# Kernel tuning notes

Measured on AMD Instinct MI355X. Metric: run time of the kernel, lower is better.

Reference implementation:

```python
import jax, jax.numpy as jnp
import numpy as np

ALPHA_MEM = 0.95      # util.decayconst(tau_mem)
ALPHA_MEM_OUT = 0.95  # util.decayconst(tau_mem_out)
ALPHA_P = 0.99        # util.decayconst(tau_p)
SURR_SCALE = 100.0

@jax.custom_vjp
def spike(x):
    # Heaviside forward, surrogate gradient backward (SurrGradSpike)
    return (x > 0).astype(x.dtype)

def _spike_fwd(x):
    return spike(x), x

def _spike_bwd(x, g):
    return (g / (SURR_SCALE * jnp.abs(x) + 1.0) ** 2,)

spike.defvjp(_spike_fwd, _spike_bwd)


def setup_inputs() -> dict:
    B, T, N, NIN, NOUT, D = 64, 400, 1024, 128, 32, 3
    key = jax.random.key(0)
    ks = jax.random.split(key, 8)
    inputs = jax.random.normal(ks[0], (B, T, NIN), dtype=jnp.float32)
    w = jax.random.normal(ks[1], (N, N), dtype=jnp.float32) / np.sqrt(N).astype(np.float32)
    w_in = jax.random.normal(ks[2], (NIN, N), dtype=jnp.float32) * np.float32(0.3 / np.sqrt(NIN))
    w_out = jax.random.normal(ks[3], (N, NOUT), dtype=jnp.float32) * np.float32(0.3 / np.sqrt(N))
    w_signs = jnp.where(jax.random.uniform(ks[4], (N,)) < 0.8, 1.0, -1.0).astype(jnp.float32)
    dmap = (jax.random.uniform(ks[5], (D, N, N)) < 0.2).astype(jnp.float32)  # delay-wise connectivity mask
    p = jax.random.uniform(ks[6], (N,), minval=-0.5, maxval=0.5).astype(jnp.float32)
    delays = jnp.array([1, 2, 4], dtype=jnp.int32)
    return dict(inputs=inputs, w=w, w_in=w_in, w_out=w_out, w_signs=w_signs,
                dmap=dmap, p=p, delays=delays)


def _forward(inputs, w, w_in, w_out, w_signs, dmap, p, delays):
    B, T, _ = inputs.shape
    N = w.shape[0]
    L = int(np.max(np.asarray(delays))) + 1  # ring-buffer length (static)
    dtype = inputs.dtype

    inp = jnp.einsum('btc,cn->btn', inputs, w_in)           # epoch.input, (B,T,N)
    W = dmap * (w_signs[:, None] * jnp.abs(w))[None]        # (D,N,N)
    depr = (p < 0).astype(dtype)                            # p_depr_mask

    def step(carry, inp_t):
        mem, w_p, buf_out, buf_wp, t = carry
        out = spike(mem - 1.0)                              # mark_spikes
        buf_out = buf_out.at[t % L].set(out)                # record_state
        buf_wp = buf_wp.at[t % L].set(w_p)
        idx = (t - delays) % L
        syn_p = buf_out[idx] * (1.0 + buf_wp[idx])          # (D,B,N)
        syn = jnp.einsum('dbe,deo->bo', syn_p, W)
        w_p_new = w_p * ALPHA_P + out * p * (1.0 + depr * w_p)
        mem_new = ALPHA_MEM * mem + inp_t + syn - jax.lax.stop_gradient(out)
        return (mem_new, w_p_new, buf_out, buf_wp, t + 1), out

    z = jnp.zeros((B, N), dtype)
    bufs = jnp.zeros((L, B, N), dtype)
    carry0 = (z, z, bufs, bufs, jnp.int32(0))
    _, out_rec = jax.lax.scan(step, carry0, jnp.swapaxes(inp, 0, 1))  # (T,B,N)

    # compute_readout: leaky integrator over projected spikes
    h2 = jnp.einsum('tbn,no->tbo', out_rec, w_out)
    def ro_step(r, h):
        r = ALPHA_MEM_OUT * r + h
        return r, r
    _, readout = jax.lax.scan(ro_step, jnp.zeros((B, w_out.shape[1]), dtype), h2)
    return jnp.swapaxes(readout, 0, 1)                      # (B,T,NOUT)


def reference(inputs, w, w_in, w_out, w_signs, dmap, p, delays):
    return _forward(inputs, w, w_in, w_out, w_signs, dmap, p, delays)
```

## Files before the change

### kernel.cpp

```cpp
#include <hip/hip_runtime.h>
#include <cstdint>
#include <cstddef>

#define BB    64
#define TT    400
#define NN    1024
#define NIN   128
#define NOUT  32
#define DD    3
#define LL6   6
#define GG    16
#define BPG   4
#define NT    32
#define KK    3072

#define ALPHA_MEM     0.95f
#define ALPHA_MEM_OUT 0.95f
#define ALPHA_P       0.99f

__global__ void build_W(const float* __restrict__ w,
                        const float* __restrict__ w_signs,
                        const float* __restrict__ dmap,
                        float* __restrict__ W) {
    int idx = blockIdx.x * blockDim.x + threadIdx.x;
    if (idx >= DD * NN * NN) return;
    int en = idx % (NN * NN);
    int e  = en / NN;
    W[idx] = dmap[idx] * (w_signs[e] * fabsf(w[en]));
}

__global__ void gemm_in(const float* __restrict__ inputs,
                        const float* __restrict__ w_in,
                        float* __restrict__ inp) {
    int idx = blockIdx.x * blockDim.x + threadIdx.x;
    if (idx >= TT * BB * NN) return;
    int n  = idx & (NN - 1);
    int tb = idx >> 10;
    int b  = tb & 63;
    int t  = tb >> 6;
    const float* row = inputs + ((size_t)b * TT + t) * NIN;
    float acc = 0.0f;
    #pragma unroll 8
    for (int c = 0; c < NIN; ++c)
        acc = fmaf(row[c], w_in[c * NN + n], acc);
    inp[idx] = acc;
}

__global__ void zero_sc1(float* __restrict__ p, int n) {
    int i = blockIdx.x * blockDim.x + threadIdx.x;
    if (i < n)
        __hip_atomic_store(p + i, 0.0f, __ATOMIC_RELAXED, __HIP_MEMORY_SCOPE_AGENT);
}

__global__ __launch_bounds__(256, 2) void snn_scan(
    const float* __restrict__ inputs,
    const float* __restrict__ w_in,
    const float* __restrict__ w_out,
    const float* __restrict__ p,
    const int*   __restrict__ delays,
    const float* __restrict__ W,
    const float* __restrict__ w_raw,
    const float* __restrict__ w_signs,
    const float* __restrict__ dmap,
    float*       __restrict__ ring,
    int*         __restrict__ cnt,
    float*       __restrict__ hpart,
    const float* __restrict__ inp_pre,
    float*       __restrict__ out,
    int use_pre, int use_W)
{
    __shared__ __align__(16) float sa[KK * BPG];
    __shared__ float w_out_s[32 * NOUT];
    __shared__ float spk_s[BPG * 32];
    __shared__ float s_sign[NN];
    __shared__ float s_in[BPG * NIN];

    const int bid  = blockIdx.x;
    const int g    = bid >> 5;
    const int tile = bid & 31;
    const int tid  = threadIdx.x;
    const int lane = tid & 63;
    const int wv   = tid >> 6;

    const bool st = (tid < BPG * 32);
    const int  sb = tid >> 5;
    const int  nl = tid & 31;

    const int gks = tid >> 3;
    const int gcg = tid & 7;

    float mem = 0.0f, wp = 0.0f, r = 0.0f;
    float pn = 0.0f, depr = 0.0f;
    if (st) { pn = p[tile * 32 + nl]; depr = (pn < 0.0f) ? 1.0f : 0.0f; }

    const int d0 = delays[0], d1 = delays[1], d2 = delays[2];

    for (int k = tid; k < 32 * NOUT; k += 256)
        w_out_s[k] = w_out[(tile * 32 + (k >> 5)) * NOUT + (k & 31)];
    if (!use_W)
        for (int k = tid; k < NN; k += 256) s_sign[k] = w_signs[k];
    __syncthreads();

    const float* Wt = W     + tile * 32 + gcg * 4;
    const float* Dt = dmap  + tile * 32 + gcg * 4;
    const float* Rt = w_raw + tile * 32 + gcg * 4;

    for (int t = 0; t < TT; ++t) {
        const int slot_w = t % LL6;
        const int s0 = (t - d0 + 2 * LL6) % LL6;
        const int s1 = (t - d1 + 2 * LL6) % LL6;
        const int s2 = (t - d2 + 2 * LL6) % LL6;

        bool  spk = false;
        float ia  = 0.0f;
        if (st) {
            spk = (mem - 1.0f) > 0.0f;
            const float a = spk ? (1.0f + wp) : 0.0f;
            __hip_atomic_store(ring + (((size_t)slot_w * BB + g * BPG + sb) << 10)
                                    + tile * 32 + nl,
                               a, __ATOMIC_RELAXED, __HIP_MEMORY_SCOPE_AGENT);
            wp = ALPHA_P * wp + (spk ? pn * (1.0f + depr * wp) : 0.0f);
            spk_s[tid] = spk ? 1.0f : 0.0f;
            if (use_pre)
                ia = inp_pre[((size_t)t * BB + g * BPG + sb) * NN + tile * 32 + nl];
        }
        if (!use_pre) {
            for (int k = tid; k < BPG * NIN; k += 256) {
                int b2 = k >> 7, c = k & 127;
                s_in[k] = inputs[((size_t)(g * BPG + b2) * TT + t) * NIN + c];
            }
        }
        __syncthreads();

        if (st) {
            float h = 0.0f;
            #pragma unroll
            for (int n2 = 0; n2 < 32; ++n2)
                h = fmaf(spk_s[sb * 32 + n2], w_out_s[n2 * 32 + nl], h);
            __hip_atomic_store(hpart + ((((size_t)(t & 1) * NT + tile) * BB)
                                        + g * BPG + sb) * NOUT + nl,
                               h, __ATOMIC_RELAXED, __HIP_MEMORY_SCOPE_AGENT);
            if (!use_pre) {
                #pragma unroll 8
                for (int c = 0; c < NIN; ++c)
                    ia = fmaf(s_in[sb * NIN + c], w_in[c * NN + tile * 32 + nl], ia);
            }
        }
        __syncthreads();

        if (tid == 0) {
            __hip_atomic_fetch_add(&cnt[g * 32], 1, __ATOMIC_RELEASE,
                                   __HIP_MEMORY_SCOPE_AGENT);
            const int target = 32 * (t + 1);
            while (__hip_atomic_load(&cnt[g * 32], __ATOMIC_RELAXED,
                                     __HIP_MEMORY_SCOPE_AGENT) < target)
                __builtin_amdgcn_s_sleep(2);
        }
        __syncthreads();

        if (tile == 0 && st) {
            float h = 0.0f;
            #pragma unroll
            for (int k3 = 0; k3 < NT; ++k3)
                h += __hip_atomic_load(hpart + ((((size_t)(t & 1) * NT + k3) * BB)
                                                + g * BPG + sb) * NOUT + nl,
                                       __ATOMIC_RELAXED, __HIP_MEMORY_SCOPE_AGENT);
            r = ALPHA_MEM_OUT * r + h;
            out[((size_t)(g * BPG + sb) * TT + t) * NOUT + nl] = r;
        }

        {
            const int b2 = lane >> 4;
            const int eo = lane & 15;
            #pragma unroll 16
            for (int i = 0; i < 48; ++i) {
                const int c  = i * 4 + wv;
                const int kl = c * 16 + eo;
                const int d  = kl >> 10;
                const int e  = kl & 1023;
                const int sl = (d == 0) ? s0 : ((d == 1) ? s1 : s2);
                const float v = __hip_atomic_load(
                    ring + (((size_t)sl * BB + g * BPG + b2) << 10) + e,
                    __ATOMIC_RELAXED, __HIP_MEMORY_SCOPE_AGENT);
                sa[kl * 4 + b2] = v;
            }
        }
        __syncthreads();

        float4 acc0 = {0,0,0,0}, acc1 = {0,0,0,0}, acc2 = {0,0,0,0}, acc3 = {0,0,0,0};
        if (use_W) {
            #pragma unroll 8
            for (int i = 0; i < 96; ++i) {
                const int kk = gks + (i << 5);
                const float4 av = *(const float4*)&sa[kk << 2];
                const float4 wv4 = *(const float4*)(Wt + ((size_t)kk << 10));
                acc0.x = fmaf(av.x, wv4.x, acc0.x); acc0.y = fmaf(av.x, wv4.y, acc0.y);
                acc0.z = fmaf(av.x, wv4.z, acc0.z); acc0.w = fmaf(av.x, wv4.w, acc0.w);
                acc1.x = fmaf(av.y, wv4.x, acc1.x); acc1.y = fmaf(av.y, wv4.y, acc1.y);
                acc1.z = fmaf(av.y, wv4.z, acc1.z); acc1.w = fmaf(av.y, wv4.w, acc1.w);
                acc2.x = fmaf(av.z, wv4.x, acc2.x); acc2.y = fmaf(av.z, wv4.y, acc2.y);
                acc2.z = fmaf(av.z, wv4.z, acc2.z); acc2.w = fmaf(av.z, wv4.w, acc2.w);
                acc3.x = fmaf(av.w, wv4.x, acc3.x); acc3.y = fmaf(av.w, wv4.y, acc3.y);
                acc3.z = fmaf(av.w, wv4.z, acc3.z); acc3.w = fmaf(av.w, wv4.w, acc3.w);
            }
        } else {
            #pragma unroll 2
            for (int i = 0; i < 96; ++i) {
                const int kk = gks + (i << 5);
                const int e  = kk & 1023;
                const float sg = s_sign[e];
                const float4 dm = *(const float4*)(Dt + ((size_t)kk << 10));
                const float4 wr = *(const float4*)(Rt + ((size_t)e << 10));
                float4 wv4;
                wv4.x = dm.x * (sg * fabsf(wr.x));
                wv4.y = dm.y * (sg * fabsf(wr.y));
                wv4.z = dm.z * (sg * fabsf(wr.z));
                wv4.w = dm.w * (sg * fabsf(wr.w));
                const float4 av = *(const float4*)&sa[kk << 2];
                acc0.x = fmaf(av.x, wv4.x, acc0.x); acc0.y = fmaf(av.x, wv4.y, acc0.y);
                acc0.z = fmaf(av.x, wv4.z, acc0.z); acc0.w = fmaf(av.x, wv4.w, acc0.w);
                acc1.x = fmaf(av.y, wv4.x, acc1.x); acc1.y = fmaf(av.y, wv4.y, acc1.y);
                acc1.z = fmaf(av.y, wv4.z, acc1.z); acc1.w = fmaf(av.y, wv4.w, acc1.w);
                acc2.x = fmaf(av.z, wv4.x, acc2.x); acc2.y = fmaf(av.z, wv4.y, acc2.y);
                acc2.z = fmaf(av.z, wv4.z, acc2.z); acc2.w = fmaf(av.z, wv4.w, acc2.w);
                acc3.x = fmaf(av.w, wv4.x, acc3.x); acc3.y = fmaf(av.w, wv4.y, acc3.y);
                acc3.z = fmaf(av.w, wv4.z, acc3.z); acc3.w = fmaf(av.w, wv4.w, acc3.w);
            }
        }
        __syncthreads();

        float* red = sa;
        {
            const int o0 = gcg * 4;
            red[(0 * 32 + o0 + 0) * 33 + gks] = acc0.x;
            red[(0 * 32 + o0 + 1) * 33 + gks] = acc0.y;
            red[(0 * 32 + o0 + 2) * 33 + gks] = acc0.z;
            red[(0 * 32 + o0 + 3) * 33 + gks] = acc0.w;
            red[(1 * 32 + o0 + 0) * 33 + gks] = acc1.x;
            red[(1 * 32 + o0 + 1) * 33 + gks] = acc1.y;
            red[(1 * 32 + o0 + 2) * 33 + gks] = acc1.z;
            red[(1 * 32 + o0 + 3) * 33 + gks] = acc1.w;
            red[(2 * 32 + o0 + 0) * 33 + gks] = acc2.x;
            red[(2 * 32 + o0 + 1) * 33 + gks] = acc2.y;
            red[(2 * 32 + o0 + 2) * 33 + gks] = acc2.z;
            red[(2 * 32 + o0 + 3) * 33 + gks] = acc2.w;
            red[(3 * 32 + o0 + 0) * 33 + gks] = acc3.x;
            red[(3 * 32 + o0 + 1) * 33 + gks] = acc3.y;
            red[(3 * 32 + o0 + 2) * 33 + gks] = acc3.z;
            red[(3 * 32 + o0 + 3) * 33 + gks] = acc3.w;
        }
        __syncthreads();

        if (st) {
            float syn = 0.0f;
            #pragma unroll
            for (int k2 = 0; k2 < 32; ++k2)
                syn += red[tid * 33 + k2];
            mem = ALPHA_MEM * mem + ia + syn - (spk ? 1.0f : 0.0f);
        }
        __syncthreads();
    }
}

extern "C" void kernel_launch(void* const* d_in, const int* in_sizes, int n_in,
                              void* d_out, int out_size, void* d_ws, size_t ws_size,
                              hipStream_t stream) {
    const float* inputs  = (const float*)d_in[0];
    const float* w       = (const float*)d_in[1];
    const float* w_in    = (const float*)d_in[2];
    const float* w_out   = (const float*)d_in[3];
    const float* w_signs = (const float*)d_in[4];
    const float* dmap    = (const float*)d_in[5];
    const float* p       = (const float*)d_in[6];
    const int*   delays  = (const int*)d_in[7];
    float*       outp    = (float*)d_out;

    const size_t ring_f = (size_t)LL6 * BB * NN;
    const size_t cnt_f  = GG * 32;
    const size_t hp_f   = (size_t)2 * NT * BB * NOUT;
    const size_t W_f    = (size_t)DD * NN * NN;
    const size_t pre_f  = (size_t)TT * BB * NN;

    float* ws = (float*)d_ws;
    float* ring  = ws;
    int*   cntp  = (int*)(ws + ring_f);
    float* hpart = ws + ring_f + cnt_f;
    size_t used  = ring_f + cnt_f + hp_f;

    int use_W = 0, use_pre = 0;
    float *W = nullptr, *inp_pre = nullptr;
    if (ws_size >= (used + W_f) * 4)   { use_W = 1;   W = ws + used;       used += W_f; }
    if (ws_size >= (used + pre_f) * 4) { use_pre = 1; inp_pre = ws + used; used += pre_f; }

    if (use_W) {
        const int total = DD * NN * NN;
        build_W<<<(total + 255) / 256, 256, 0, stream>>>(w, w_signs, dmap, W);
    }
    if (use_pre) {
        const int total = TT * BB * NN;
        gemm_in<<<(total + 255) / 256, 256, 0, stream>>>(inputs, w_in, inp_pre);
    }
    {
        const int total = (int)(ring_f + cnt_f);
        zero_sc1<<<(total + 255) / 256, 256, 0, stream>>>(ring, total);
    }

    void* args[] = {
        (void*)&inputs, (void*)&w_in, (void*)&w_out, (void*)&p, (void*)&delays,
        (void*)&W, (void*)&w, (void*)&w_signs, (void*)&dmap,
        (void*)&ring, (void*)&cntp, (void*)&hpart, (void*)&inp_pre, (void*)&outp,
        (void*)&use_pre, (void*)&use_W
    };
    hipError_t cerr = hipLaunchCooperativeKernel((const void*)snn_scan,
                               dim3(GG * NT), dim3(256), args, 0, stream);
    if (cerr != hipSuccess) {
        hipLaunchKernelGGL(snn_scan, dim3(GG * NT), dim3(256), 0, stream,
                           inputs, w_in, w_out, p, delays, W, w, w_signs, dmap,
                           ring, cntp, hpart, inp_pre, outp, use_pre, use_W);
    }
}
```

Baseline: 11.36 ms.

## Defer grid barrier wait past matvec and software-pipeline W loads

Moves the inter-block spin-wait from before the synaptic matvec to the end of each timestep, so the barrier latency overlaps with the matvec. The readout reduction is delayed by one step, and the partial-sum buffer grows to three slots so the deferred reads stay safe. It also batches all ring-buffer loads into registers before the shared-memory stores, and double-buffers the W float4 loads in groups of eight to hide global latency. The trade-off is higher register pressure under launch_bounds(256,2), plus a subtle memory-ordering dependency on the deferred barrier.

New measurement: 15.63 ms. 1.38x slower.

```diff
diff --git a/kernel.cpp b/kernel.cpp
--- a/kernel.cpp
+++ b/kernel.cpp
@@ -51,6 +51,17 @@
     if (i < n)
         __hip_atomic_store(p + i, 0.0f, __ATOMIC_RELAXED, __HIP_MEMORY_SCOPE_AGENT);
 }
+
+#define FMA16(av, wv4) do { \
+    acc0.x = fmaf(av.x, wv4.x, acc0.x); acc0.y = fmaf(av.x, wv4.y, acc0.y); \
+    acc0.z = fmaf(av.x, wv4.z, acc0.z); acc0.w = fmaf(av.x, wv4.w, acc0.w); \
+    acc1.x = fmaf(av.y, wv4.x, acc1.x); acc1.y = fmaf(av.y, wv4.y, acc1.y); \
+    acc1.z = fmaf(av.y, wv4.z, acc1.z); acc1.w = fmaf(av.y, wv4.w, acc1.w); \
+    acc2.x = fmaf(av.z, wv4.x, acc2.x); acc2.y = fmaf(av.z, wv4.y, acc2.y); \
+    acc2.z = fmaf(av.z, wv4.z, acc2.z); acc2.w = fmaf(av.z, wv4.w, acc2.w); \
+    acc3.x = fmaf(av.w, wv4.x, acc3.x); acc3.y = fmaf(av.w, wv4.y, acc3.y); \
+    acc3.z = fmaf(av.w, wv4.z, acc3.z); acc3.w = fmaf(av.w, wv4.w, acc3.w); \
+} while (0)
 
 __global__ __launch_bounds__(256, 2) void snn_scan(
     const float* __restrict__ inputs,
@@ -137,7 +148,7 @@
             #pragma unroll
             for (int n2 = 0; n2 < 32; ++n2)
                 h = fmaf(spk_s[sb * 32 + n2], w_out_s[n2 * 32 + nl], h);
-            __hip_atomic_store(hpart + ((((size_t)(t & 1) * NT + tile) * BB)
+            __hip_atomic_store(hpart + ((((size_t)(t % 3) * NT + tile) * BB)
                                         + g * BPG + sb) * NOUT + nl,
                                h, __ATOMIC_RELAXED, __HIP_MEMORY_SCOPE_AGENT);
             if (!use_pre) {
@@ -148,60 +159,71 @@
         }
         __syncthreads();
 
-        if (tid == 0) {
+        if (tid == 0)
             __hip_atomic_fetch_add(&cnt[g * 32], 1, __ATOMIC_RELEASE,
                                    __HIP_MEMORY_SCOPE_AGENT);
-            const int target = 32 * (t + 1);
-            while (__hip_atomic_load(&cnt[g * 32], __ATOMIC_RELAXED,
-                                     __HIP_MEMORY_SCOPE_AGENT) < target)
-                __builtin_amdgcn_s_sleep(2);
-        }
-        __syncthreads();
-
-        if (tile == 0 && st) {
+
+        if (tile == 0 && st && t > 0) {
+            const int tp = (t - 1) % 3;
             float h = 0.0f;
             #pragma unroll
             for (int k3 = 0; k3 < NT; ++k3)
-                h += __hip_atomic_load(hpart + ((((size_t)(t & 1) * NT + k3) * BB)
+                h += __hip_atomic_load(hpart + ((((size_t)tp * NT + k3) * BB)
                                                 + g * BPG + sb) * NOUT + nl,
                                        __ATOMIC_RELAXED, __HIP_MEMORY_SCOPE_AGENT);
             r = ALPHA_MEM_OUT * r + h;
-            out[((size_t)(g * BPG + sb) * TT + t) * NOUT + nl] = r;
+            out[((size_t)(g * BPG + sb) * TT + (t - 1)) * NOUT + nl] = r;
         }
 
         {
             const int b2 = lane >> 4;
             const int eo = lane & 15;
-            #pragma unroll 16
+            float va[48];
+            #pragma unroll
             for (int i = 0; i < 48; ++i) {
                 const int c  = i * 4 + wv;
                 const int kl = c * 16 + eo;
                 const int d  = kl >> 10;
                 const int e  = kl & 1023;
                 const int sl = (d == 0) ? s0 : ((d == 1) ? s1 : s2);
-                const float v = __hip_atomic_load(
+                va[i] = __hip_atomic_load(
                     ring + (((size_t)sl * BB + g * BPG + b2) << 10) + e,
                     __ATOMIC_RELAXED, __HIP_MEMORY_SCOPE_AGENT);
-                sa[kl * 4 + b2] = v;
+            }
+            #pragma unroll
+            for (int i = 0; i < 48; ++i) {
+                const int kl = (i * 4 + wv) * 16 + eo;
+                sa[kl * 4 + b2] = va[i];
             }
         }
         __syncthreads();
 
         float4 acc0 = {0,0,0,0}, acc1 = {0,0,0,0}, acc2 = {0,0,0,0}, acc3 = {0,0,0,0};
         if (use_W) {
-            #pragma unroll 8
-            for (int i = 0; i < 96; ++i) {
-                const int kk = gks + (i << 5);
-                const float4 av = *(const float4*)&sa[kk << 2];
-                const float4 wv4 = *(const float4*)(Wt + ((size_t)kk << 10));
-                acc0.x = fmaf(av.x, wv4.x, acc0.x); acc0.y = fmaf(av.x, wv4.y, acc0.y);
-                acc0.z = fmaf(av.x, wv4.z, acc0.z); acc0.w = fmaf(av.x, wv4.w, acc0.w);
-                acc1.x = fmaf(av.y, wv4.x, acc1.x); acc1.y = fmaf(av.y, wv4.y, acc1.y);
-                acc1.z = fmaf(av.y, wv4.z, acc1.z); acc1.w = fmaf(av.y, wv4.w, acc1.w);
-                acc2.x = fmaf(av.z, wv4.x, acc2.x); acc2.y = fmaf(av.z, wv4.y, acc2.y);
-                acc2.z = fmaf(av.z, wv4.z, acc2.z); acc2.w = fmaf(av.z, wv4.w, acc2.w);
-                acc3.x = fmaf(av.w, wv4.x, acc3.x); acc3.y = fmaf(av.w, wv4.y, acc3.y);
-                acc3.z = fmaf(av.w, wv4.z, acc3.z); acc3.w = fmaf(av.w, wv4.w, acc3.w);
+            float4 wbuf[8];
+            #pragma unroll
+            for (int j = 0; j < 8; ++j)
+                wbuf[j] = *(const float4*)(Wt + ((size_t)(gks + (j << 5)) << 10));
+            #pragma unroll 1
+            for (int i8 = 0; i8 < 12; ++i8) {
+                float4 wnext[8];
+                if (i8 < 11) {
+                    #pragma unroll
+                    for (int j = 0; j < 8; ++j)
+                        wnext[j] = *(const float4*)(Wt +
+                            ((size_t)(gks + (((i8 + 1) * 8 + j) << 5)) << 10));
+                }
+                #pragma unroll
+                for (int j = 0; j < 8; ++j) {
+                    const int kk = gks + ((i8 * 8 + j) << 5);
+                    const float4 av  = *(const float4*)&sa[kk << 2];
+                    const float4 wv4 = wbuf[j];
+                    FMA16(av, wv4);
+                }
+                if (i8 < 11) {
+                    #pragma unroll
+                    for (int j = 0; j < 8; ++j) wbuf[j] = wnext[j];
+                }
             }
         } else {
             #pragma unroll 2
@@ -217,14 +239,7 @@
                 wv4.z = dm.z * (sg * fabsf(wr.z));
                 wv4.w = dm.w * (sg * fabsf(wr.w));
                 const float4 av = *(const float4*)&sa[kk << 2];
-                acc0.x = fmaf(av.x, wv4.x, acc0.x); acc0.y = fmaf(av.x, wv4.y, acc0.y);
-                acc0.z = fmaf(av.x, wv4.z, acc0.z); acc0.w = fmaf(av.x, wv4.w, acc0.w);
-                acc1.x = fmaf(av.y, wv4.x, acc1.x); acc1.y = fmaf(av.y, wv4.y, acc1.y);
-                acc1.z = fmaf(av.y, wv4.z, acc1.z); acc1.w = fmaf(av.y, wv4.w, acc1.w);
-                acc2.x = fmaf(av.z, wv4.x, acc2.x); acc2.y = fmaf(av.z, wv4.y, acc2.y);
-                acc2.z = fmaf(av.z, wv4.z, acc2.z); acc2.w = fmaf(av.z, wv4.w, acc2.w);
-                acc3.x = fmaf(av.w, wv4.x, acc3.x); acc3.y = fmaf(av.w, wv4.y, acc3.y);
-                acc3.z = fmaf(av.w, wv4.z, acc3.z); acc3.w = fmaf(av.w, wv4.w, acc3.w);
+                FMA16(av, wv4);
             }
         }
         __syncthreads();
@@ -259,6 +274,26 @@
             mem = ALPHA_MEM * mem + ia + syn - (spk ? 1.0f : 0.0f);
         }
         __syncthreads();
+
+        if (tid == 0) {
+            const int target = 32 * (t + 1);
+            while (__hip_atomic_load(&cnt[g * 32], __ATOMIC_ACQUIRE,
+                                     __HIP_MEMORY_SCOPE_AGENT) < target)
+                __builtin_amdgcn_s_sleep(2);
+        }
+        __syncthreads();
+    }
+
+    if (tile == 0 && st) {
+        const int tp = (TT - 1) % 3;
+        float h = 0.0f;
+        #pragma unroll
+        for (int k3 = 0; k3 < NT; ++k3)
+            h += __hip_atomic_load(hpart + ((((size_t)tp * NT + k3) * BB)
+                                            + g * BPG + sb) * NOUT + nl,
+                                   __ATOMIC_RELAXED, __HIP_MEMORY_SCOPE_AGENT);
+        r = ALPHA_MEM_OUT * r + h;
+        out[((size_t)(g * BPG + sb) * TT + (TT - 1)) * NOUT + nl] = r;
     }
 }
 
@@ -277,7 +312,7 @@
 
     const size_t ring_f = (size_t)LL6 * BB * NN;
     const size_t cnt_f  = GG * 32;
-    const size_t hp_f   = (size_t)2 * NT * BB * NOUT;
+    const size_t hp_f   = (size_t)3 * NT * BB * NOUT;
     const size_t W_f    = (size_t)DD * NN * NN;
     const size_t pre_f  = (size_t)TT * BB * NN;
 
```
